# Optimization experiments

Hardware: AMD Instinct MI355X
Metric: run time of the kernel (lower is better)

The kernel has to match this reference:

```python
import jax, jax.numpy as jnp
import numpy as np

B, T, N, D = 2, 16, 512, 256
HID, HEADS = 256, 8
HD = HID // HEADS // 2  # 16
SCALE = HD ** -0.5
LAMBDA_INIT = 0.8 - 0.6 * float(np.exp(-0.3 * (2 - 1)))  # layer_idx = 2
LN_EPS = 1e-5


def setup_inputs() -> dict:
    key = jax.random.key(0)
    ks = jax.random.split(key, 8)
    return {
        "x": jax.random.normal(ks[0], (B, T, N, D), dtype=jnp.float32),
        "Wq": jax.random.normal(ks[1], (D, HID), dtype=jnp.float32) * (D ** -0.5),
        "Wk": jax.random.normal(ks[2], (D, HID), dtype=jnp.float32) * (D ** -0.5),
        "Wv": jax.random.normal(ks[3], (D, HID), dtype=jnp.float32) * (D ** -0.5),
        "lq1": jax.random.normal(ks[4], (HD,), dtype=jnp.float32) * 0.1,
        "lk1": jax.random.normal(ks[5], (HD,), dtype=jnp.float32) * 0.1,
        "lq2": jax.random.normal(ks[6], (HD,), dtype=jnp.float32) * 0.1,
        "lk2": jax.random.normal(ks[7], (HD,), dtype=jnp.float32) * 0.1,
        "ln_gamma": jnp.ones((2 * HD,), dtype=jnp.float32),
        "ln_beta": jnp.zeros((2 * HD,), dtype=jnp.float32),
    }


def _attn_pair(q, k, v1, v2):
    # q,k,v*: [BT, N, H, HD]; shared softmax applied to both value halves
    p = jax.nn.softmax(jnp.einsum('bnhd,bmhd->bhnm', q, k) * SCALE, axis=-1)
    o1 = jnp.einsum('bhnm,bmhd->bnhd', p, v1)
    o2 = jnp.einsum('bhnm,bmhd->bnhd', p, v2)
    return jnp.concatenate([o1, o2], axis=-1)  # [BT, N, H, 2*HD]


def reference(x, Wq, Wk, Wv, lq1, lk1, lq2, lk2, ln_gamma, ln_beta):
    b, t, n, d = x.shape
    # 1x1 Conv2d over channel dim == per-token linear projection
    q = jnp.einsum('btnd,dh->btnh', x, Wq).reshape(b * t, n, HEADS, 2 * HD)
    k = jnp.einsum('btnd,dh->btnh', x, Wk).reshape(b * t, n, HEADS, 2 * HD)
    v = jnp.einsum('btnd,dh->btnh', x, Wv).reshape(b * t, n, HEADS, 2 * HD)
    q1, q2 = jnp.split(q, 2, axis=-1)
    k1, k2 = jnp.split(k, 2, axis=-1)
    v1, v2 = jnp.split(v, 2, axis=-1)
    attn1 = _attn_pair(q1, k1, v1, v2)
    attn2 = _attn_pair(q2, k2, v1, v2)
    lam = jnp.exp(jnp.sum(lq1 * lk1)) - jnp.exp(jnp.sum(lq2 * lk2)) + LAMBDA_INIT
    y = attn1 - lam * attn2  # [BT, N, H, 2*HD]
    mu = jnp.mean(y, axis=-1, keepdims=True)
    var = jnp.mean(jnp.square(y - mu), axis=-1, keepdims=True)
    y = (y - mu) * jax.lax.rsqrt(var + LN_EPS) * ln_gamma + ln_beta
    y = y * (1.0 - LAMBDA_INIT)
    return y.reshape(b, t, n, HEADS * 2 * HD)
```

## Files before the change

### kernel.cpp

```cpp
#include <hip/hip_runtime.h>
#include <cmath>

typedef unsigned short u16;
typedef unsigned int   u32;
typedef __attribute__((ext_vector_type(8))) short short8;
typedef __attribute__((ext_vector_type(4))) float f32x4;

constexpr int BT    = 32;
constexpr int NTOK  = 512;
constexpr int DIM   = 256;
constexpr int HID   = 256;
constexpr int M_ROWS = BT * NTOK;
constexpr float SCALE = 0.25f;
constexpr float LAMBDA_INIT  = 0.35550906759096927f;
constexpr float ONE_MINUS_LI = 0.6444909324090307f;
constexpr float LN_EPS = 1e-5f;

#define MFMA16(a, b, c) __builtin_amdgcn_mfma_f32_16x16x32_bf16((a), (b), (c), 0, 0, 0)

__device__ __forceinline__ u16 f2bf(float f) {
    u32 u = __float_as_uint(f);
    u32 r = (u + 0x7FFFu + ((u >> 16) & 1u)) >> 16;
    return (u16)r;
}

__device__ __forceinline__ short8 ldb64x2(const u16* p) {
    uint2 a = *(const uint2*)p;
    uint2 b = *(const uint2*)(p + 4);
    union { u32 u[4]; short8 s; } x;
    x.u[0] = a.x; x.u[1] = a.y; x.u[2] = b.x; x.u[3] = b.y;
    return x.s;
}

__global__ __launch_bounds__(256) void prep_x(const float* __restrict__ x, u16* __restrict__ xb) {
    size_t i = ((size_t)blockIdx.x * 256 + threadIdx.x) * 8;
    float4 a = *(const float4*)&x[i];
    float4 b = *(const float4*)&x[i + 4];
    uint4 o;
    o.x = (u32)f2bf(a.x) | ((u32)f2bf(a.y) << 16);
    o.y = (u32)f2bf(a.z) | ((u32)f2bf(a.w) << 16);
    o.z = (u32)f2bf(b.x) | ((u32)f2bf(b.y) << 16);
    o.w = (u32)f2bf(b.z) | ((u32)f2bf(b.w) << 16);
    *(uint4*)&xb[i] = o;
}

__global__ __launch_bounds__(256) void prep_w(const float* __restrict__ Wq,
                                              const float* __restrict__ Wk,
                                              const float* __restrict__ Wv,
                                              u16* __restrict__ Wt) {
    const float* W = (blockIdx.z == 0) ? Wq : (blockIdx.z == 1) ? Wk : Wv;
    u16* dst = Wt + (size_t)blockIdx.z * 65536;
    __shared__ float T[64][65];
    const int k0 = blockIdx.x * 64, n0 = blockIdx.y * 64;
    const int tr = threadIdx.x >> 4;
    const int tc = threadIdx.x & 15;
    #pragma unroll
    for (int i = 0; i < 4; ++i) {
        int row = tr + i * 16;
        float4 v = *(const float4*)&W[(size_t)(k0 + row) * HID + n0 + tc * 4];
        T[row][tc * 4 + 0] = v.x; T[row][tc * 4 + 1] = v.y;
        T[row][tc * 4 + 2] = v.z; T[row][tc * 4 + 3] = v.w;
    }
    __syncthreads();
    #pragma unroll
    for (int i = 0; i < 4; ++i) {
        int n = tr + i * 16;
        int k4 = tc * 4;
        uint2 pk;
        pk.x = (u32)f2bf(T[k4 + 0][n]) | ((u32)f2bf(T[k4 + 1][n]) << 16);
        pk.y = (u32)f2bf(T[k4 + 2][n]) | ((u32)f2bf(T[k4 + 3][n]) << 16);
        *(uint2*)&dst[(size_t)(n0 + n) * DIM + k0 + k4] = pk;
    }
}

__global__ __launch_bounds__(256, 2) void proj_kernel(
    const u16* __restrict__ xb, const u16* __restrict__ Wt,
    u16* __restrict__ Qb, u16* __restrict__ Kb, u16* __restrict__ Vb)
{
    const int z = blockIdx.z;
    const u16* Wz = Wt + (size_t)z * 65536;
    u16* C = (z == 0) ? Qb : (z == 1) ? Kb : Vb;

    __shared__ u16 As[64 * 40];
    __shared__ u16 Bs[64 * 40];

    const int tid  = threadIdx.x;
    const int m0   = blockIdx.x * 64;
    const int n0   = blockIdx.y * 64;
    const int lane = tid & 63;
    const int wv   = tid >> 6;
    const int q16  = lane & 15;
    const int quad = lane >> 4;
    const int mw   = (wv >> 1) * 32;
    const int nw   = (wv & 1) * 32;

    const int sr = tid >> 2;
    const int sc = (tid & 3) * 8;

    f32x4 acc00 = {0.f,0.f,0.f,0.f}, acc01 = {0.f,0.f,0.f,0.f};
    f32x4 acc10 = {0.f,0.f,0.f,0.f}, acc11 = {0.f,0.f,0.f,0.f};

    for (int kk = 0; kk < DIM; kk += 32) {
        *(uint4*)&As[sr * 40 + sc] = *(const uint4*)&xb[(size_t)(m0 + sr) * DIM + kk + sc];
        *(uint4*)&Bs[sr * 40 + sc] = *(const uint4*)&Wz[(size_t)(n0 + sr) * DIM + kk + sc];
        __syncthreads();

        short8 a0 = *(const short8*)&As[(mw +      q16) * 40 + quad * 8];
        short8 a1 = *(const short8*)&As[(mw + 16 + q16) * 40 + quad * 8];
        short8 b0 = *(const short8*)&Bs[(nw +      q16) * 40 + quad * 8];
        short8 b1 = *(const short8*)&Bs[(nw + 16 + q16) * 40 + quad * 8];

        acc00 = MFMA16(a0, b0, acc00);
        acc01 = MFMA16(a0, b1, acc01);
        acc10 = MFMA16(a1, b0, acc10);
        acc11 = MFMA16(a1, b1, acc11);
        __syncthreads();
    }

    #pragma unroll
    for (int r = 0; r < 4; ++r) {
        const int row0 = m0 + mw + quad * 4 + r;
        const int col0 = n0 + nw + q16;
        C[(size_t)row0 * HID + col0]            = f2bf(acc00[r]);
        C[(size_t)row0 * HID + col0 + 16]       = f2bf(acc01[r]);
        C[(size_t)(row0 + 16) * HID + col0]     = f2bf(acc10[r]);
        C[(size_t)(row0 + 16) * HID + col0 + 16] = f2bf(acc11[r]);
    }
}

__global__ __launch_bounds__(256, 2) void attn_kernel(
    const u16* __restrict__ Qb, const u16* __restrict__ Kb, const u16* __restrict__ Vb,
    const float* __restrict__ lq1, const float* __restrict__ lk1,
    const float* __restrict__ lq2, const float* __restrict__ lk2,
    const float* __restrict__ gamma, const float* __restrict__ beta,
    float* __restrict__ out)
{
    __shared__ u16 Ks[512 * 36];
    __shared__ u16 Vts[32 * 520];
    __shared__ u16 Pbuf[4][2][16 * 36];

    const int qh = blockIdx.x;
    const int h  = blockIdx.y;
    const int bt = blockIdx.z;
    const int tid = threadIdx.x;

    {
        const u16* Kg = Kb + ((size_t)bt * NTOK) * HID + h * 32;
        #pragma unroll
        for (int p = 0; p < 2; ++p) {
            const int rr = tid + p * 256;
            const uint4* src = (const uint4*)(Kg + (size_t)rr * HID);
            u16* dst = &Ks[rr * 36];
            #pragma unroll
            for (int i = 0; i < 4; ++i) {
                uint4 v = src[i];
                uint2 w0; w0.x = v.x; w0.y = v.y;
                uint2 w1; w1.x = v.z; w1.y = v.w;
                *(uint2*)(dst + i * 8)     = w0;
                *(uint2*)(dst + i * 8 + 4) = w1;
            }
        }
    }
    {
        const u16* Vg = Vb + ((size_t)bt * NTOK) * HID + h * 32;
        const int j0 = tid * 2;
        union { uint4 q[4]; u16 us[32]; } ra, rb;
        const uint4* s0 = (const uint4*)(Vg + (size_t)j0 * HID);
        const uint4* s1 = (const uint4*)(Vg + (size_t)(j0 + 1) * HID);
        #pragma unroll
        for (int i = 0; i < 4; ++i) { ra.q[i] = s0[i]; rb.q[i] = s1[i]; }
        #pragma unroll
        for (int d = 0; d < 32; ++d) {
            u32 val = (u32)ra.us[d] | ((u32)rb.us[d] << 16);
            *(u32*)&Vts[d * 520 + j0] = val;
        }
    }
    __syncthreads();

    float sa = 0.f, sb = 0.f;
    #pragma unroll
    for (int d = 0; d < 16; ++d) { sa += lq1[d] * lk1[d]; sb += lq2[d] * lk2[d]; }
    const float lam = __expf(sa) - __expf(sb) + LAMBDA_INIT;

    const int lane = tid & 63;
    const int wv   = tid >> 6;
    const int q16  = lane & 15;
    const int quad = lane >> 4;

    const float g_lo = gamma[q16],      g_hi = gamma[16 + q16];
    const float b_lo = beta[q16],       b_hi = beta[16 + q16];

    u16* P1 = &Pbuf[wv][0][0];
    u16* P2 = &Pbuf[wv][1][0];

    const short8 z8 = {0,0,0,0,0,0,0,0};
    const f32x4  z4 = {0.f,0.f,0.f,0.f};

    for (int qb = wv; qb < 16; qb += 4) {
        const int qrow = bt * NTOK + qh * 256 + qb * 16 + q16;
        short8 qv = *(const short8*)(Qb + (size_t)qrow * HID + h * 32 + quad * 8);
        short8 A1 = (lane < 32) ? qv : z8;
        short8 A2 = (lane < 32) ? z8 : qv;

        f32x4 o1lo = z4, o1hi = z4, o2lo = z4, o2hi = z4;
        float l1p[4] = {0.f,0.f,0.f,0.f};
        float l2p[4] = {0.f,0.f,0.f,0.f};

        for (int kc = 0; kc < 16; ++kc) {
            #pragma unroll
            for (int sub = 0; sub < 2; ++sub) {
                const int key0 = kc * 32 + sub * 16;
                short8 kf = ldb64x2(&Ks[(key0 + q16) * 36 + quad * 8]);
                f32x4 s1 = MFMA16(A1, kf, z4);
                f32x4 s2 = MFMA16(A2, kf, z4);
                #pragma unroll
                for (int r = 0; r < 4; ++r) {
                    float p1 = __expf(s1[r] * SCALE);
                    float p2 = __expf(s2[r] * SCALE);
                    l1p[r] += p1; l2p[r] += p2;
                    P1[(quad * 4 + r) * 36 + sub * 16 + q16] = f2bf(p1);
                    P2[(quad * 4 + r) * 36 + sub * 16 + q16] = f2bf(p2);
                }
            }
            short8 pf1 = ldb64x2(&P1[q16 * 36 + quad * 8]);
            short8 pf2 = ldb64x2(&P2[q16 * 36 + quad * 8]);
            short8 vlo = *(const short8*)&Vts[q16 * 520 + kc * 32 + quad * 8];
            short8 vhi = *(const short8*)&Vts[(16 + q16) * 520 + kc * 32 + quad * 8];
            o1lo = MFMA16(pf1, vlo, o1lo);
            o1hi = MFMA16(pf1, vhi, o1hi);
            o2lo = MFMA16(pf2, vlo, o2lo);
            o2hi = MFMA16(pf2, vhi, o2hi);
        }

        #pragma unroll
        for (int r = 0; r < 4; ++r) {
            float a = l1p[r], b = l2p[r];
            #pragma unroll
            for (int off = 1; off < 16; off <<= 1) {
                a += __shfl_xor(a, off);
                b += __shfl_xor(b, off);
            }
            l1p[r] = a; l2p[r] = b;
        }

        #pragma unroll
        for (int r = 0; r < 4; ++r) {
            const float inv1 = 1.0f / l1p[r];
            const float inv2 = 1.0f / l2p[r];
            const float ylo = o1lo[r] * inv1 - lam * (o2lo[r] * inv2);
            const float yhi = o1hi[r] * inv1 - lam * (o2hi[r] * inv2);

            float s  = ylo + yhi;
            float s2 = ylo * ylo + yhi * yhi;
            #pragma unroll
            for (int off = 1; off < 16; off <<= 1) {
                s  += __shfl_xor(s,  off);
                s2 += __shfl_xor(s2, off);
            }
            const float mu   = s * (1.0f / 32.0f);
            const float var  = s2 * (1.0f / 32.0f) - mu * mu;
            const float rstd = rsqrtf(var + LN_EPS);

            const int row = bt * NTOK + qh * 256 + qb * 16 + quad * 4 + r;
            float* orow = out + (size_t)row * HID + h * 32;
            orow[q16]      = ((ylo - mu) * rstd * g_lo + b_lo) * ONE_MINUS_LI;
            orow[16 + q16] = ((yhi - mu) * rstd * g_hi + b_hi) * ONE_MINUS_LI;
        }
    }
}

extern "C" void kernel_launch(void* const* d_in, const int* in_sizes, int n_in,
                              void* d_out, int out_size, void* d_ws, size_t ws_size,
                              hipStream_t stream) {
    const float* x   = (const float*)d_in[0];
    const float* Wq  = (const float*)d_in[1];
    const float* Wk  = (const float*)d_in[2];
    const float* Wv  = (const float*)d_in[3];
    const float* lq1 = (const float*)d_in[4];
    const float* lk1 = (const float*)d_in[5];
    const float* lq2 = (const float*)d_in[6];
    const float* lk2 = (const float*)d_in[7];
    const float* gam = (const float*)d_in[8];
    const float* bet = (const float*)d_in[9];
    float* out = (float*)d_out;

    u16* ws = (u16*)d_ws;
    u16* xb = ws;
    u16* Wt = xb + (size_t)M_ROWS * DIM;
    u16* Qb = Wt + 3 * 256 * 256;
    u16* Kb = Qb + (size_t)M_ROWS * HID;
    u16* Vb = Kb + (size_t)M_ROWS * HID;

    hipLaunchKernelGGL(prep_x, dim3(2048), dim3(256), 0, stream, x, xb);
    hipLaunchKernelGGL(prep_w, dim3(4, 4, 3), dim3(256), 0, stream, Wq, Wk, Wv, Wt);
    hipLaunchKernelGGL(proj_kernel, dim3(M_ROWS / 64, HID / 64, 3), dim3(256), 0, stream,
                       xb, Wt, Qb, Kb, Vb);
    hipLaunchKernelGGL(attn_kernel, dim3(2, 8, 32), dim3(256), 0, stream,
                       Qb, Kb, Vb, lq1, lk1, lq2, lk2, gam, bet, out);
}
```

Before: 160.0 us.

## Fuse x cast into QKV projection, head-major layout, chunked attention with exp2

Removes the separate prep_x pass by converting x to bf16 inside the projection kernel, which now computes Q, K and V together from one A tile with K=64 steps. Q/K/V are written head-major and Q is prescaled by scale*log2e, so attention can use exp2 directly. The attention kernel processes 128 queries per block, streams K/V in two 256-key chunks to cut LDS, transposes V with perm ops and packs P with vector stores. It also computes row sums through a transposed score layout, which needs fewer shuffles. The trade-off is more registers per thread and a larger grid, and P now uses truncation-style rounding.

```diff
diff --git a/kernel.cpp b/kernel.cpp
--- a/kernel.cpp
+++ b/kernel.cpp
@@ -11,37 +11,32 @@
 constexpr int DIM   = 256;
 constexpr int HID   = 256;
 constexpr int M_ROWS = BT * NTOK;
-constexpr float SCALE = 0.25f;
+constexpr int HM     = M_ROWS * 32;
+constexpr size_t TENS = (size_t)M_ROWS * HID;
 constexpr float LAMBDA_INIT  = 0.35550906759096927f;
 constexpr float ONE_MINUS_LI = 0.6444909324090307f;
 constexpr float LN_EPS = 1e-5f;
+constexpr float QSCALE = 0.36067376022224085f;
 
 #define MFMA16(a, b, c) __builtin_amdgcn_mfma_f32_16x16x32_bf16((a), (b), (c), 0, 0, 0)
 
 __device__ __forceinline__ u16 f2bf(float f) {
     u32 u = __float_as_uint(f);
-    u32 r = (u + 0x7FFFu + ((u >> 16) & 1u)) >> 16;
-    return (u16)r;
-}
-
-__device__ __forceinline__ short8 ldb64x2(const u16* p) {
-    uint2 a = *(const uint2*)p;
-    uint2 b = *(const uint2*)(p + 4);
-    union { u32 u[4]; short8 s; } x;
-    x.u[0] = a.x; x.u[1] = a.y; x.u[2] = b.x; x.u[3] = b.y;
-    return x.s;
-}
-
-__global__ __launch_bounds__(256) void prep_x(const float* __restrict__ x, u16* __restrict__ xb) {
-    size_t i = ((size_t)blockIdx.x * 256 + threadIdx.x) * 8;
-    float4 a = *(const float4*)&x[i];
-    float4 b = *(const float4*)&x[i + 4];
-    uint4 o;
-    o.x = (u32)f2bf(a.x) | ((u32)f2bf(a.y) << 16);
-    o.y = (u32)f2bf(a.z) | ((u32)f2bf(a.w) << 16);
-    o.z = (u32)f2bf(b.x) | ((u32)f2bf(b.y) << 16);
-    o.w = (u32)f2bf(b.z) | ((u32)f2bf(b.w) << 16);
-    *(uint4*)&xb[i] = o;
+    return (u16)((u + 0x7FFFu + ((u >> 16) & 1u)) >> 16);
+}
+
+__device__ __forceinline__ float fexp2(float x) {
+#if defined(__has_builtin) && __has_builtin(__builtin_amdgcn_exp2f)
+    return __builtin_amdgcn_exp2f(x);
+#else
+    return exp2f(x);
+#endif
+}
+
+__device__ __forceinline__ u32 pack_bf16(float a, float b) {
+    u32 ua = __float_as_uint(a) + 0x8000u;
+    u32 ub = __float_as_uint(b) + 0x8000u;
+    return __builtin_amdgcn_perm(ub, ua, 0x07060302u);
 }
 
 __global__ __launch_bounds__(256) void prep_w(const float* __restrict__ Wq,
@@ -73,16 +68,12 @@
     }
 }
 
-__global__ __launch_bounds__(256, 2) void proj_kernel(
-    const u16* __restrict__ xb, const u16* __restrict__ Wt,
-    u16* __restrict__ Qb, u16* __restrict__ Kb, u16* __restrict__ Vb)
+__global__ __launch_bounds__(256, 3) void proj_kernel(
+    const float* __restrict__ x, const u16* __restrict__ Wt,
+    u16* __restrict__ Qh, u16* __restrict__ Kh, u16* __restrict__ Vh)
 {
-    const int z = blockIdx.z;
-    const u16* Wz = Wt + (size_t)z * 65536;
-    u16* C = (z == 0) ? Qb : (z == 1) ? Kb : Vb;
-
-    __shared__ u16 As[64 * 40];
-    __shared__ u16 Bs[64 * 40];
+    __shared__ u16 As[64 * 72];
+    __shared__ u16 Bs[3][64 * 72];
 
     const int tid  = threadIdx.x;
     const int m0   = blockIdx.x * 64;
@@ -95,160 +86,194 @@
     const int nw   = (wv & 1) * 32;
 
     const int sr = tid >> 2;
-    const int sc = (tid & 3) * 8;
-
-    f32x4 acc00 = {0.f,0.f,0.f,0.f}, acc01 = {0.f,0.f,0.f,0.f};
-    f32x4 acc10 = {0.f,0.f,0.f,0.f}, acc11 = {0.f,0.f,0.f,0.f};
-
-    for (int kk = 0; kk < DIM; kk += 32) {
-        *(uint4*)&As[sr * 40 + sc] = *(const uint4*)&xb[(size_t)(m0 + sr) * DIM + kk + sc];
-        *(uint4*)&Bs[sr * 40 + sc] = *(const uint4*)&Wz[(size_t)(n0 + sr) * DIM + kk + sc];
+    const int sc = (tid & 3) * 16;
+
+    f32x4 acc[3][4];
+    #pragma unroll
+    for (int z = 0; z < 3; ++z)
+        #pragma unroll
+        for (int t = 0; t < 4; ++t)
+            acc[z][t] = (f32x4){0.f, 0.f, 0.f, 0.f};
+
+    for (int kk = 0; kk < DIM; kk += 64) {
+        {
+            const float4* xs = (const float4*)&x[(size_t)(m0 + sr) * DIM + kk + sc];
+            float4 g0 = xs[0], g1 = xs[1], g2 = xs[2], g3 = xs[3];
+            uint4 o0, o1;
+            o0.x = (u32)f2bf(g0.x) | ((u32)f2bf(g0.y) << 16);
+            o0.y = (u32)f2bf(g0.z) | ((u32)f2bf(g0.w) << 16);
+            o0.z = (u32)f2bf(g1.x) | ((u32)f2bf(g1.y) << 16);
+            o0.w = (u32)f2bf(g1.z) | ((u32)f2bf(g1.w) << 16);
+            o1.x = (u32)f2bf(g2.x) | ((u32)f2bf(g2.y) << 16);
+            o1.y = (u32)f2bf(g2.z) | ((u32)f2bf(g2.w) << 16);
+            o1.z = (u32)f2bf(g3.x) | ((u32)f2bf(g3.y) << 16);
+            o1.w = (u32)f2bf(g3.z) | ((u32)f2bf(g3.w) << 16);
+            *(uint4*)&As[sr * 72 + sc]     = o0;
+            *(uint4*)&As[sr * 72 + sc + 8] = o1;
+        }
+        #pragma unroll
+        for (int z = 0; z < 3; ++z) {
+            const uint4* ws4 = (const uint4*)&Wt[(size_t)z * 65536 + (size_t)(n0 + sr) * DIM + kk + sc];
+            *(uint4*)&Bs[z][sr * 72 + sc]     = ws4[0];
+            *(uint4*)&Bs[z][sr * 72 + sc + 8] = ws4[1];
+        }
         __syncthreads();
-
-        short8 a0 = *(const short8*)&As[(mw +      q16) * 40 + quad * 8];
-        short8 a1 = *(const short8*)&As[(mw + 16 + q16) * 40 + quad * 8];
-        short8 b0 = *(const short8*)&Bs[(nw +      q16) * 40 + quad * 8];
-        short8 b1 = *(const short8*)&Bs[(nw + 16 + q16) * 40 + quad * 8];
-
-        acc00 = MFMA16(a0, b0, acc00);
-        acc01 = MFMA16(a0, b1, acc01);
-        acc10 = MFMA16(a1, b0, acc10);
-        acc11 = MFMA16(a1, b1, acc11);
+        #pragma unroll
+        for (int kc = 0; kc < 2; ++kc) {
+            short8 a0 = *(const short8*)&As[(mw +      q16) * 72 + kc * 32 + quad * 8];
+            short8 a1 = *(const short8*)&As[(mw + 16 + q16) * 72 + kc * 32 + quad * 8];
+            #pragma unroll
+            for (int z = 0; z < 3; ++z) {
+                short8 b0 = *(const short8*)&Bs[z][(nw +      q16) * 72 + kc * 32 + quad * 8];
+                short8 b1 = *(const short8*)&Bs[z][(nw + 16 + q16) * 72 + kc * 32 + quad * 8];
+                acc[z][0] = MFMA16(a0, b0, acc[z][0]);
+                acc[z][1] = MFMA16(a0, b1, acc[z][1]);
+                acc[z][2] = MFMA16(a1, b0, acc[z][2]);
+                acc[z][3] = MFMA16(a1, b1, acc[z][3]);
+            }
+        }
         __syncthreads();
     }
 
-    #pragma unroll
-    for (int r = 0; r < 4; ++r) {
-        const int row0 = m0 + mw + quad * 4 + r;
-        const int col0 = n0 + nw + q16;
-        C[(size_t)row0 * HID + col0]            = f2bf(acc00[r]);
-        C[(size_t)row0 * HID + col0 + 16]       = f2bf(acc01[r]);
-        C[(size_t)(row0 + 16) * HID + col0]     = f2bf(acc10[r]);
-        C[(size_t)(row0 + 16) * HID + col0 + 16] = f2bf(acc11[r]);
-    }
-}
-
-__global__ __launch_bounds__(256, 2) void attn_kernel(
-    const u16* __restrict__ Qb, const u16* __restrict__ Kb, const u16* __restrict__ Vb,
+    const int hcol = (n0 + nw) >> 5;
+    #pragma unroll
+    for (int z = 0; z < 3; ++z) {
+        u16* C = (z == 0) ? Qh : (z == 1) ? Kh : Vh;
+        u16* base = C + (size_t)hcol * HM;
+        const float s = (z == 0) ? QSCALE : 1.0f;
+        #pragma unroll
+        for (int r = 0; r < 4; ++r) {
+            const int row = m0 + mw + quad * 4 + r;
+            base[(size_t)row * 32 + q16]             = f2bf(acc[z][0][r] * s);
+            base[(size_t)row * 32 + q16 + 16]        = f2bf(acc[z][1][r] * s);
+            base[(size_t)(row + 16) * 32 + q16]      = f2bf(acc[z][2][r] * s);
+            base[(size_t)(row + 16) * 32 + q16 + 16] = f2bf(acc[z][3][r] * s);
+        }
+    }
+}
+
+__global__ __launch_bounds__(256, 3) void attn_kernel(
+    const u16* __restrict__ Qh, const u16* __restrict__ Kh, const u16* __restrict__ Vh,
     const float* __restrict__ lq1, const float* __restrict__ lk1,
     const float* __restrict__ lq2, const float* __restrict__ lk2,
     const float* __restrict__ gamma, const float* __restrict__ beta,
     float* __restrict__ out)
 {
-    __shared__ u16 Ks[512 * 36];
-    __shared__ u16 Vts[32 * 520];
-    __shared__ u16 Pbuf[4][2][16 * 36];
-
-    const int qh = blockIdx.x;
-    const int h  = blockIdx.y;
-    const int bt = blockIdx.z;
+    __shared__ u16 Ks[256 * 40];
+    __shared__ u16 Vts[32 * 264];
+    __shared__ u16 Pbuf[4][2][16 * 40];
+
+    const int qh  = blockIdx.x;
+    const int h   = blockIdx.y;
+    const int bt  = blockIdx.z;
     const int tid = threadIdx.x;
-
-    {
-        const u16* Kg = Kb + ((size_t)bt * NTOK) * HID + h * 32;
-        #pragma unroll
-        for (int p = 0; p < 2; ++p) {
-            const int rr = tid + p * 256;
-            const uint4* src = (const uint4*)(Kg + (size_t)rr * HID);
-            u16* dst = &Ks[rr * 36];
-            #pragma unroll
-            for (int i = 0; i < 4; ++i) {
-                uint4 v = src[i];
-                uint2 w0; w0.x = v.x; w0.y = v.y;
-                uint2 w1; w1.x = v.z; w1.y = v.w;
-                *(uint2*)(dst + i * 8)     = w0;
-                *(uint2*)(dst + i * 8 + 4) = w1;
-            }
-        }
-    }
-    {
-        const u16* Vg = Vb + ((size_t)bt * NTOK) * HID + h * 32;
-        const int j0 = tid * 2;
-        union { uint4 q[4]; u16 us[32]; } ra, rb;
-        const uint4* s0 = (const uint4*)(Vg + (size_t)j0 * HID);
-        const uint4* s1 = (const uint4*)(Vg + (size_t)(j0 + 1) * HID);
-        #pragma unroll
-        for (int i = 0; i < 4; ++i) { ra.q[i] = s0[i]; rb.q[i] = s1[i]; }
-        #pragma unroll
-        for (int d = 0; d < 32; ++d) {
-            u32 val = (u32)ra.us[d] | ((u32)rb.us[d] << 16);
-            *(u32*)&Vts[d * 520 + j0] = val;
-        }
-    }
-    __syncthreads();
-
-    float sa = 0.f, sb = 0.f;
-    #pragma unroll
-    for (int d = 0; d < 16; ++d) { sa += lq1[d] * lk1[d]; sb += lq2[d] * lk2[d]; }
-    const float lam = __expf(sa) - __expf(sb) + LAMBDA_INIT;
-
     const int lane = tid & 63;
     const int wv   = tid >> 6;
     const int q16  = lane & 15;
     const int quad = lane >> 4;
 
+    float sa = 0.f, sb = 0.f;
+    #pragma unroll
+    for (int d = 0; d < 16; ++d) { sa += lq1[d] * lk1[d]; sb += lq2[d] * lk2[d]; }
+    const float lam = __expf(sa) - __expf(sb) + LAMBDA_INIT;
+
+    short8 qv[2];
+    #pragma unroll
+    for (int qbi = 0; qbi < 2; ++qbi) {
+        const int qrow = bt * NTOK + qh * 128 + (qbi * 4 + wv) * 16 + q16;
+        qv[qbi] = *(const short8*)(Qh + (size_t)h * HM + (size_t)qrow * 32 + quad * 8);
+    }
+
+    const short8 z8 = {0, 0, 0, 0, 0, 0, 0, 0};
+    const f32x4  z4 = {0.f, 0.f, 0.f, 0.f};
+
+    f32x4 o1lo[2], o1hi[2], o2lo[2], o2hi[2];
+    #pragma unroll
+    for (int qbi = 0; qbi < 2; ++qbi) {
+        o1lo[qbi] = z4; o1hi[qbi] = z4; o2lo[qbi] = z4; o2hi[qbi] = z4;
+    }
+    float l1[2] = {0.f, 0.f}, l2[2] = {0.f, 0.f};
+
+    u16* P1 = &Pbuf[wv][0][0];
+    u16* P2 = &Pbuf[wv][1][0];
+
+    for (int chunk = 0; chunk < 2; ++chunk) {
+        if (chunk) __syncthreads();
+        {
+            const uint4* src = (const uint4*)(Kh + (size_t)h * HM +
+                                (size_t)(bt * NTOK + chunk * 256 + tid) * 32);
+            uint4* dst = (uint4*)&Ks[tid * 40];
+            dst[0] = src[0]; dst[1] = src[1]; dst[2] = src[2]; dst[3] = src[3];
+        }
+        if (tid < 128) {
+            const int j0 = tid * 2;
+            const u16* v0 = Vh + (size_t)h * HM + (size_t)(bt * NTOK + chunk * 256 + j0) * 32;
+            union U { uint4 q[4]; u32 w[16]; } ra, rb;
+            #pragma unroll
+            for (int i = 0; i < 4; ++i) {
+                ra.q[i] = ((const uint4*)v0)[i];
+                rb.q[i] = ((const uint4*)(v0 + 32))[i];
+            }
+            #pragma unroll
+            for (int w = 0; w < 16; ++w) {
+                u32 lo = __builtin_amdgcn_perm(rb.w[w], ra.w[w], 0x05040100u);
+                u32 hi = __builtin_amdgcn_perm(rb.w[w], ra.w[w], 0x07060302u);
+                *(u32*)&Vts[(2 * w)     * 264 + j0] = lo;
+                *(u32*)&Vts[(2 * w + 1) * 264 + j0] = hi;
+            }
+        }
+        __syncthreads();
+
+        #pragma unroll
+        for (int qbi = 0; qbi < 2; ++qbi) {
+            const short8 A1 = (lane < 32) ? qv[qbi] : z8;
+            const short8 A2 = (lane < 32) ? z8 : qv[qbi];
+            for (int kc = 0; kc < 8; ++kc) {
+                #pragma unroll
+                for (int sub = 0; sub < 2; ++sub) {
+                    const int key0 = kc * 32 + sub * 16;
+                    short8 kf = *(const short8*)&Ks[(key0 + q16) * 40 + quad * 8];
+                    f32x4 s1 = MFMA16(kf, A1, z4);
+                    f32x4 s2 = MFMA16(kf, A2, z4);
+                    float p0 = fexp2(s1[0]), p1 = fexp2(s1[1]);
+                    float p2 = fexp2(s1[2]), p3 = fexp2(s1[3]);
+                    l1[qbi] += (p0 + p1) + (p2 + p3);
+                    uint2 w1; w1.x = pack_bf16(p0, p1); w1.y = pack_bf16(p2, p3);
+                    *(uint2*)&P1[q16 * 40 + sub * 16 + quad * 4] = w1;
+                    float r0 = fexp2(s2[0]), r1 = fexp2(s2[1]);
+                    float r2 = fexp2(s2[2]), r3 = fexp2(s2[3]);
+                    l2[qbi] += (r0 + r1) + (r2 + r3);
+                    uint2 w2; w2.x = pack_bf16(r0, r1); w2.y = pack_bf16(r2, r3);
+                    *(uint2*)&P2[q16 * 40 + sub * 16 + quad * 4] = w2;
+                }
+                short8 pf1 = *(const short8*)&P1[q16 * 40 + quad * 8];
+                short8 pf2 = *(const short8*)&P2[q16 * 40 + quad * 8];
+                short8 vlo = *(const short8*)&Vts[q16        * 264 + kc * 32 + quad * 8];
+                short8 vhi = *(const short8*)&Vts[(16 + q16) * 264 + kc * 32 + quad * 8];
+                o1lo[qbi] = MFMA16(pf1, vlo, o1lo[qbi]);
+                o1hi[qbi] = MFMA16(pf1, vhi, o1hi[qbi]);
+                o2lo[qbi] = MFMA16(pf2, vlo, o2lo[qbi]);
+                o2hi[qbi] = MFMA16(pf2, vhi, o2hi[qbi]);
+            }
+        }
+    }
+
     const float g_lo = gamma[q16],      g_hi = gamma[16 + q16];
     const float b_lo = beta[q16],       b_hi = beta[16 + q16];
 
-    u16* P1 = &Pbuf[wv][0][0];
-    u16* P2 = &Pbuf[wv][1][0];
-
-    const short8 z8 = {0,0,0,0,0,0,0,0};
-    const f32x4  z4 = {0.f,0.f,0.f,0.f};
-
-    for (int qb = wv; qb < 16; qb += 4) {
-        const int qrow = bt * NTOK + qh * 256 + qb * 16 + q16;
-        short8 qv = *(const short8*)(Qb + (size_t)qrow * HID + h * 32 + quad * 8);
-        short8 A1 = (lane < 32) ? qv : z8;
-        short8 A2 = (lane < 32) ? z8 : qv;
-
-        f32x4 o1lo = z4, o1hi = z4, o2lo = z4, o2hi = z4;
-        float l1p[4] = {0.f,0.f,0.f,0.f};
-        float l2p[4] = {0.f,0.f,0.f,0.f};
-
-        for (int kc = 0; kc < 16; ++kc) {
-            #pragma unroll
-            for (int sub = 0; sub < 2; ++sub) {
-                const int key0 = kc * 32 + sub * 16;
-                short8 kf = ldb64x2(&Ks[(key0 + q16) * 36 + quad * 8]);
-                f32x4 s1 = MFMA16(A1, kf, z4);
-                f32x4 s2 = MFMA16(A2, kf, z4);
-                #pragma unroll
-                for (int r = 0; r < 4; ++r) {
-                    float p1 = __expf(s1[r] * SCALE);
-                    float p2 = __expf(s2[r] * SCALE);
-                    l1p[r] += p1; l2p[r] += p2;
-                    P1[(quad * 4 + r) * 36 + sub * 16 + q16] = f2bf(p1);
-                    P2[(quad * 4 + r) * 36 + sub * 16 + q16] = f2bf(p2);
-                }
-            }
-            short8 pf1 = ldb64x2(&P1[q16 * 36 + quad * 8]);
-            short8 pf2 = ldb64x2(&P2[q16 * 36 + quad * 8]);
-            short8 vlo = *(const short8*)&Vts[q16 * 520 + kc * 32 + quad * 8];
-            short8 vhi = *(const short8*)&Vts[(16 + q16) * 520 + kc * 32 + quad * 8];
-            o1lo = MFMA16(pf1, vlo, o1lo);
-            o1hi = MFMA16(pf1, vhi, o1hi);
-            o2lo = MFMA16(pf2, vlo, o2lo);
-            o2hi = MFMA16(pf2, vhi, o2hi);
-        }
-
+    #pragma unroll
+    for (int qbi = 0; qbi < 2; ++qbi) {
+        float a = l1[qbi], b = l2[qbi];
+        a += __shfl_xor(a, 16); a += __shfl_xor(a, 32);
+        b += __shfl_xor(b, 16); b += __shfl_xor(b, 32);
+        const float inv1 = 1.0f / a;
+        const float inv2 = 1.0f / b;
         #pragma unroll
         for (int r = 0; r < 4; ++r) {
-            float a = l1p[r], b = l2p[r];
-            #pragma unroll
-            for (int off = 1; off < 16; off <<= 1) {
-                a += __shfl_xor(a, off);
-                b += __shfl_xor(b, off);
-            }
-            l1p[r] = a; l2p[r] = b;
-        }
-
-        #pragma unroll
-        for (int r = 0; r < 4; ++r) {
-            const float inv1 = 1.0f / l1p[r];
-            const float inv2 = 1.0f / l2p[r];
-            const float ylo = o1lo[r] * inv1 - lam * (o2lo[r] * inv2);
-            const float yhi = o1hi[r] * inv1 - lam * (o2hi[r] * inv2);
+            const float i1 = __shfl(inv1, quad * 4 + r);
+            const float i2 = __shfl(inv2, quad * 4 + r);
+            const float ylo = o1lo[qbi][r] * i1 - lam * (o2lo[qbi][r] * i2);
+            const float yhi = o1hi[qbi][r] * i1 - lam * (o2hi[qbi][r] * i2);
 
             float s  = ylo + yhi;
             float s2 = ylo * ylo + yhi * yhi;
@@ -261,7 +286,7 @@
             const float var  = s2 * (1.0f / 32.0f) - mu * mu;
             const float rstd = rsqrtf(var + LN_EPS);
 
-            const int row = bt * NTOK + qh * 256 + qb * 16 + quad * 4 + r;
+            const int row = bt * NTOK + qh * 128 + (qbi * 4 + wv) * 16 + quad * 4 + r;
             float* orow = out + (size_t)row * HID + h * 32;
             orow[q16]      = ((ylo - mu) * rstd * g_lo + b_lo) * ONE_MINUS_LI;
             orow[16 + q16] = ((yhi - mu) * rstd * g_hi + b_hi) * ONE_MINUS_LI;
@@ -285,16 +310,14 @@
     float* out = (float*)d_out;
 
     u16* ws = (u16*)d_ws;
-    u16* xb = ws;
-    u16* Wt = xb + (size_t)M_ROWS * DIM;
-    u16* Qb = Wt + 3 * 256 * 256;
-    u16* Kb = Qb + (size_t)M_ROWS * HID;
-    u16* Vb = Kb + (size_t)M_ROWS * HID;
-
-    hipLaunchKernelGGL(prep_x, dim3(2048), dim3(256), 0, stream, x, xb);
+    u16* Wt = ws;
+    u16* Qh = Wt + 3 * 65536;
+    u16* Kh = Qh + TENS;
+    u16* Vh = Kh + TENS;
+
     hipLaunchKernelGGL(prep_w, dim3(4, 4, 3), dim3(256), 0, stream, Wq, Wk, Wv, Wt);
-    hipLaunchKernelGGL(proj_kernel, dim3(M_ROWS / 64, HID / 64, 3), dim3(256), 0, stream,
-                       xb, Wt, Qb, Kb, Vb);
-    hipLaunchKernelGGL(attn_kernel, dim3(2, 8, 32), dim3(256), 0, stream,
-                       Qb, Kb, Vb, lq1, lk1, lq2, lk2, gam, bet, out);
-}
+    hipLaunchKernelGGL(proj_kernel, dim3(M_ROWS / 64, HID / 64), dim3(256), 0, stream,
+                       x, Wt, Qh, Kh, Vh);
+    hipLaunchKernelGGL(attn_kernel, dim3(4, 8, 32), dim3(256), 0, stream,
+                       Qh, Kh, Vh, lq1, lk1, lq2, lk2, gam, bet, out);
+}
```

Result: faster. 134.3 us (-16.1%).
